# Kernel optimization log

Hardware: AMD Instinct MI355X
Metric: run time of the kernel (lower is better)

Reference implementation:

```python
import jax, jax.numpy as jnp
import numpy as np

N = 100000
IN_DIM = 128
HID = 64
OUT = 4


def _gcn_conv(x, W, b, src, dst, deg_inv_sqrt):
    """PyG GCNConv: linear transform, then symmetric-normalized scatter-add.
    src/dst already include self-loops; deg_inv_sqrt precomputed over them."""
    h = x @ W                                   # [N, H]
    norm = deg_inv_sqrt[src] * deg_inv_sqrt[dst]  # [E+N]
    msg = h[src] * norm[:, None]                # gather + scale, [E+N, H]
    out = jax.ops.segment_sum(msg, dst, num_segments=N)  # scatter-add
    return out + b


def setup_inputs() -> dict:
    key = jax.random.key(0)
    ks = jax.random.split(key, 8)
    E = 1600000
    x = jax.random.normal(ks[0], (N, IN_DIM), dtype=jnp.float32)
    edge_index = jax.random.randint(ks[1], (2, E), 0, N, dtype=jnp.int32)
    # Glorot-ish init for weights
    W1 = jax.random.normal(ks[2], (IN_DIM, HID), dtype=jnp.float32) / np.sqrt(IN_DIM)
    b1 = jnp.zeros((HID,), dtype=jnp.float32)
    W2 = jax.random.normal(ks[3], (HID, HID), dtype=jnp.float32) / np.sqrt(HID)
    b2 = jnp.zeros((HID,), dtype=jnp.float32)
    Wfc = jax.random.normal(ks[4], (HID, OUT), dtype=jnp.float32) / np.sqrt(HID)
    bfc = jnp.zeros((OUT,), dtype=jnp.float32)
    return {"x": x, "edge_index": edge_index, "W1": W1, "b1": b1,
            "W2": W2, "b2": b2, "Wfc": Wfc, "bfc": bfc}


def reference(x, edge_index, W1, b1, W2, b2, Wfc, bfc):
    # Add self-loops (GCNConv default add_self_loops=True)
    loops = jnp.arange(N, dtype=edge_index.dtype)
    src = jnp.concatenate([edge_index[0], loops])
    dst = jnp.concatenate([edge_index[1], loops])
    # Symmetric normalization: deg computed at aggregation targets (dst)
    deg = jax.ops.segment_sum(jnp.ones_like(dst, dtype=x.dtype), dst,
                              num_segments=N)
    deg_inv_sqrt = jnp.where(deg > 0, jax.lax.rsqrt(deg), 0.0)

    h = _gcn_conv(x, W1, b1, src, dst, deg_inv_sqrt)
    h = jax.nn.relu(h)                 # dropout is identity in eval mode
    h = _gcn_conv(h, W2, b2, src, dst, deg_inv_sqrt)
    h = jax.nn.relu(h)
    return h @ Wfc + bfc               # [N, 4]
```

## Files before the change

kernel.cpp:

```cpp
#include <hip/hip_runtime.h>
#include <hip/hip_fp16.h>


#define BCAP 5120
#define BINB 512
#define CHUNK 3200

typedef float v2f __attribute__((ext_vector_type(2)));
typedef _Float16 f16x8 __attribute__((ext_vector_type(8)));
typedef float f32x4 __attribute__((ext_vector_type(4)));

__global__ __launch_bounds__(256) void k_prep(const float* __restrict__ W1,
                                              const float* __restrict__ W2,
                                              _Float16* __restrict__ wt1,
                                              _Float16* __restrict__ wt2,
                                              int* __restrict__ bcur) {
    int gid = threadIdx.x + blockIdx.x * blockDim.x;
    {
        int k = gid >> 6, nn = gid & 63;
        wt1[nn * 136 + k] = (_Float16)W1[gid];
    }
    if (gid < 64 * 64) {
        int k = gid >> 6, nn = gid & 63;
        wt2[nn * 72 + k] = (_Float16)W2[gid];
    }
    if (gid < 512) bcur[gid] = 0;
}

__global__ __launch_bounds__(256) void k_bin(const int* __restrict__ src,
                                             const int* __restrict__ dst, int e,
                                             int* bcur, unsigned* __restrict__ binned) {
    __shared__ unsigned ec[CHUNK];
    __shared__ unsigned short eb[CHUNK];
    __shared__ int lh[512], lbase[512], lr[512];
    int t = threadIdx.x;
    for (int i = t; i < 512; i += 256) { lh[i] = 0; lr[i] = 0; }
    __syncthreads();
    int chunk = (e + gridDim.x - 1) / gridDim.x;
    int lo = blockIdx.x * chunk;
    int hi = min(e, lo + chunk);
    for (int i = lo + t; i < hi; i += 256) {
        int d = dst[i];
        int b = d >> 8;
        ec[i - lo] = ((unsigned)src[i] << 8) | (unsigned)(d & 255);
        eb[i - lo] = (unsigned short)b;
        atomicAdd(&lh[b], 1);
    }
    __syncthreads();
    for (int i = t; i < 512; i += 256)
        lbase[i] = lh[i] ? atomicAdd(&bcur[i], lh[i]) : 0;
    __syncthreads();
    int cnt = hi - lo;
    for (int i = t; i < cnt; i += 256) {
        int b = eb[i];
        int r = lbase[b] + atomicAdd(&lr[b], 1);
        if (r < BCAP)
            binned[(size_t)b * BCAP + r] = ec[i];
    }
}

__global__ __launch_bounds__(256) void k_bucket(const unsigned* __restrict__ binned,
                                                const int* __restrict__ bcur,
                                                int n, int* __restrict__ offs,
                                                int* __restrict__ cnt,
                                                float* __restrict__ dis,
                                                int* __restrict__ csr) {
    __shared__ unsigned ec[BCAP];
    __shared__ int nh[256], nsc[256], nr[256];
    int b = blockIdx.x, t = threadIdx.x;
    int node0 = b << 8;
    size_t ebase = (size_t)b * BCAP;
    int ecnt = min(bcur[b], BCAP);
    nh[t] = 0; nr[t] = 0;
    __syncthreads();
    for (int j = t; j < ecnt; j += 256) {
        unsigned ed = binned[ebase + j];
        ec[j] = ed;
        atomicAdd(&nh[ed & 255u], 1);
    }
    __syncthreads();
    int v = nh[t];
    nsc[t] = v;
    __syncthreads();
    for (int o = 1; o < 256; o <<= 1) {
        int x = (t >= o) ? nsc[t - o] : 0;
        __syncthreads();
        nsc[t] += x;
        __syncthreads();
    }
    int ex = nsc[t] - v;
    int d = node0 + t;
    if (d < n) {
        offs[d] = (int)ebase + ex;
        cnt[d]  = v;
        dis[d]  = rsqrtf((float)(v + 1));
    }
    nsc[t] = ex;
    __syncthreads();
    for (int j = t; j < ecnt; j += 256) {
        unsigned ed = ec[j];
        int ld = ed & 255u;
        int r = atomicAdd(&nr[ld], 1);
        csr[ebase + nsc[ld] + r] = (int)(ed >> 8);
    }
}

template<int K, typename TI>
__global__ __launch_bounds__(256) void k_gemm_mfma(const TI* __restrict__ X,
                                                   const _Float16* __restrict__ Wt,
                                                   const float* __restrict__ dis,
                                                   __half* __restrict__ Hh, int n) {
    constexpr int KP = K + 8;
    __shared__ _Float16 As[128 * KP];
    __shared__ _Float16 Bs[64 * KP];

    int t = threadIdx.x;
    _Float16* H = (_Float16*)Hh;

    constexpr int NF4 = 64 * KP / 8;
    for (int i = t; i < NF4; i += 256)
        ((float4*)Bs)[i] = ((const float4*)Wt)[i];

    int row0 = blockIdx.x * 128;
    if (sizeof(TI) == 4) {
        const float* Xf = (const float*)X;
        #pragma unroll
        for (int p = 0; p < 8; ++p) {
            int gi  = t + p * 256;
            int row = gi >> 4, sg = gi & 15;
            int grow = row0 + row;
            float4 v0 = make_float4(0.f, 0.f, 0.f, 0.f), v1 = v0;
            if (grow < n) {
                v0 = *(const float4*)(Xf + (size_t)grow * K + sg * 8);
                v1 = *(const float4*)(Xf + (size_t)grow * K + sg * 8 + 4);
            }
            union { __half2 h[4]; float4 f; } u;
            u.h[0] = __floats2half2_rn(v0.x, v0.y);
            u.h[1] = __floats2half2_rn(v0.z, v0.w);
            u.h[2] = __floats2half2_rn(v1.x, v1.y);
            u.h[3] = __floats2half2_rn(v1.z, v1.w);
            *(float4*)(As + row * KP + sg * 8) = u.f;
        }
    } else {
        const __half* Xh = (const __half*)X;
        #pragma unroll
        for (int p = 0; p < 4; ++p) {
            int gi  = t + p * 256;
            int row = gi >> 3, sg = gi & 7;
            int grow = row0 + row;
            float4 v = make_float4(0.f, 0.f, 0.f, 0.f);
            if (grow < n)
                v = *(const float4*)(Xh + (size_t)grow * K + sg * 8);
            *(float4*)(As + row * KP + sg * 8) = v;
        }
    }
    __syncthreads();

    int wv   = t >> 6;
    int lane = t & 63;
    int m    = lane & 15;
    int quad = lane >> 4;
    int r0   = wv * 32;

    f32x4 acc[2][4] = {};
    #pragma unroll
    for (int kb = 0; kb < K / 32; ++kb) {
        f16x8 af0 = *(const f16x8*)(As + (r0 + m) * KP + quad * 8 + kb * 32);
        f16x8 af1 = *(const f16x8*)(As + (r0 + 16 + m) * KP + quad * 8 + kb * 32);
        #pragma unroll
        for (int nt = 0; nt < 4; ++nt) {
            f16x8 bf = *(const f16x8*)(Bs + (nt * 16 + m) * KP + quad * 8 + kb * 32);
            acc[0][nt] = __builtin_amdgcn_mfma_f32_16x16x32_f16(af0, bf, acc[0][nt], 0, 0, 0);
            acc[1][nt] = __builtin_amdgcn_mfma_f32_16x16x32_f16(af1, bf, acc[1][nt], 0, 0, 0);
        }
    }

    #pragma unroll
    for (int mt = 0; mt < 2; ++mt) {
        float dv[4]; int gr[4];
        #pragma unroll
        for (int r = 0; r < 4; ++r) {
            gr[r] = row0 + r0 + mt * 16 + quad * 4 + r;
            dv[r] = (gr[r] < n) ? dis[gr[r]] : 0.f;
        }
        #pragma unroll
        for (int nt = 0; nt < 4; ++nt)
            #pragma unroll
            for (int r = 0; r < 4; ++r) {
                if (gr[r] < n)
                    H[(size_t)gr[r] * 64 + nt * 16 + m] =
                        (_Float16)(acc[mt][nt][r] * dv[r]);
                else if (gr[r] == n)
                    H[(size_t)n * 64 + nt * 16 + m] = (_Float16)0.f;
            }
    }
}

__device__ inline void add_row(const __half* __restrict__ hp, int s, int c4,
                               v2f& lo, v2f& hi) {
    float2 raw = *(const float2*)(hp + (size_t)s * 64 + c4);
    const __half2* p = (const __half2*)&raw;
    float2 l = __half22float2(p[0]);
    float2 h = __half22float2(p[1]);
    lo += (v2f){ l.x, l.y };
    hi += (v2f){ h.x, h.y };
}

template<bool FUSE>
__global__ __launch_bounds__(256) void k_gather(const __half* __restrict__ hp,
                                                const int* __restrict__ csr,
                                                const int* __restrict__ off,
                                                const int* __restrict__ cnt,
                                                const float* __restrict__ dis,
                                                const float* __restrict__ bias,
                                                void* __restrict__ outb,
                                                const float* __restrict__ Wfc,
                                                const float* __restrict__ bfc,
                                                int n) {
    int lane = threadIdx.x & 63;
    int wid  = (blockIdx.x * blockDim.x + threadIdx.x) >> 6;
    if (wid >= n) return;
    int d    = wid;
    int esub = lane >> 4;
    int c4   = (lane & 15) * 4;

    int start = off[d], num = cnt[d];
    int idx = (lane < num) ? csr[start + lane] : 0;
    int lim = min(num, 64);

    v2f aL[4] = {}, aH[4] = {};
    if (esub == 0)
        add_row(hp, d, c4, aL[0], aH[0]);

    int j = 0;
    for (; j + 16 <= lim; j += 16) {
        int s0 = __shfl(idx, j + esub);
        int s1 = __shfl(idx, j + 4 + esub);
        int s2 = __shfl(idx, j + 8 + esub);
        int s3 = __shfl(idx, j + 12 + esub);
        add_row(hp, s0, c4, aL[0], aH[0]);
        add_row(hp, s1, c4, aL[1], aH[1]);
        add_row(hp, s2, c4, aL[2], aH[2]);
        add_row(hp, s3, c4, aL[3], aH[3]);
    }
    for (; j < lim; j += 4) {
        int jj = j + esub;
        int sr = __shfl(idx, jj);
        int s  = (jj < lim) ? sr : n;
        add_row(hp, s, c4, aL[0], aH[0]);
    }
    for (int j2 = 64; j2 < num; j2 += 4) {
        int jj = j2 + esub;
        if (jj < num) {
            int s = csr[start + jj];
            add_row(hp, s, c4, aL[1], aH[1]);
        }
    }
    v2f sL = (aL[0] + aL[1]) + (aL[2] + aL[3]);
    v2f sH = (aH[0] + aH[1]) + (aH[2] + aH[3]);
    float4 a0 = make_float4(sL.x, sL.y, sH.x, sH.y);
    #pragma unroll
    for (int o = 16; o <= 32; o <<= 1) {
        a0.x += __shfl_xor(a0.x, o);
        a0.y += __shfl_xor(a0.y, o);
        a0.z += __shfl_xor(a0.z, o);
        a0.w += __shfl_xor(a0.w, o);
    }
    float dd = dis[d];
    float4 bb = *(const float4*)(bias + c4);
    float4 o;
    o.x = fmaxf(bb.x + dd * a0.x, 0.f);
    o.y = fmaxf(bb.y + dd * a0.y, 0.f);
    o.z = fmaxf(bb.z + dd * a0.z, 0.f);
    o.w = fmaxf(bb.w + dd * a0.w, 0.f);
    if (!FUSE) {
        if (esub == 0) {
            union { __half2 h[2]; float2 f; } u;
            u.h[0] = __floats2half2_rn(o.x, o.y);
            u.h[1] = __floats2half2_rn(o.z, o.w);
            *(float2*)((__half*)outb + (size_t)d * 64 + c4) = u.f;
        }
    } else {
        const float4* W4 = (const float4*)Wfc;
        float4 w0 = W4[c4 + 0], w1 = W4[c4 + 1], w2 = W4[c4 + 2], w3 = W4[c4 + 3];
        float4 p;
        p.x = o.x * w0.x + o.y * w1.x + o.z * w2.x + o.w * w3.x;
        p.y = o.x * w0.y + o.y * w1.y + o.z * w2.y + o.w * w3.y;
        p.z = o.x * w0.z + o.y * w1.z + o.z * w2.z + o.w * w3.z;
        p.w = o.x * w0.w + o.y * w1.w + o.z * w2.w + o.w * w3.w;
        #pragma unroll
        for (int q = 1; q <= 8; q <<= 1) {
            p.x += __shfl_xor(p.x, q);
            p.y += __shfl_xor(p.y, q);
            p.z += __shfl_xor(p.z, q);
            p.w += __shfl_xor(p.w, q);
        }
        if (lane == 0) {
            float4 bf = *(const float4*)bfc;
            float4 r = make_float4(p.x + bf.x, p.y + bf.y, p.z + bf.z, p.w + bf.w);
            ((float4*)outb)[d] = r;
        }
    }
}

static inline size_t align256(size_t x) { return (x + 255) & ~(size_t)255; }

extern "C" void kernel_launch(void* const* d_in, const int* in_sizes, int n_in,
                              void* d_out, int out_size, void* d_ws, size_t ws_size,
                              hipStream_t stream) {
    const float* x   = (const float*)d_in[0];
    const int*   ei  = (const int*)d_in[1];
    const float* W1  = (const float*)d_in[2];
    const float* b1  = (const float*)d_in[3];
    const float* W2  = (const float*)d_in[4];
    const float* b2  = (const float*)d_in[5];
    const float* Wfc = (const float*)d_in[6];
    const float* bfc = (const float*)d_in[7];
    float* out = (float*)d_out;

    int n = in_sizes[0] / 128;
    int e = in_sizes[1] / 2;
    const int* src = ei;
    const int* dst = ei + e;

    char* ws = (char*)d_ws;
    size_t p = 0;
    float*    dis    = (float*)   (ws + p); p = align256(p + (size_t)n * 4);
    int*      counts = (int*)     (ws + p); p = align256(p + (size_t)n * 4);
    int*      offs   = (int*)     (ws + p); p = align256(p + (size_t)n * 4);
    int*      bcur   = (int*)     (ws + p); p = align256(p + 512 * 4);
    _Float16* wt1    = (_Float16*)(ws + p); p = align256(p + 64 * 136 * 2);
    _Float16* wt2    = (_Float16*)(ws + p); p = align256(p + 64 * 72 * 2);
    int*      csr    = (int*)     (ws + p); p = align256(p + (size_t)512 * BCAP * 4);
    unsigned* binned = (unsigned*)(ws + p); p = align256(p + (size_t)512 * BCAP * 4);
    __half*   hbuf   = (__half*)  (ws + p); p = align256(p + (size_t)(n + 1) * 64 * 2);
    __half*   a1h    = (__half*)  (ws + p);

    int gb  = (n + 127) / 128;
    int nbk = (n + 255) / 256;

    k_prep<<<32, 256, 0, stream>>>(W1, W2, wt1, wt2, bcur);
    k_bin<<<BINB, 256, 0, stream>>>(src, dst, e, bcur, binned);
    k_bucket<<<nbk, 256, 0, stream>>>(binned, bcur, n, offs, counts, dis, csr);

    k_gemm_mfma<128, float><<<gb, 256, 0, stream>>>(x, wt1, dis, hbuf, n);
    k_gather<false><<<(n * 64 + 255) / 256, 256, 0, stream>>>(
        hbuf, csr, offs, counts, dis, b1, a1h, nullptr, nullptr, n);

    k_gemm_mfma<64, __half><<<gb, 256, 0, stream>>>(a1h, wt2, dis, hbuf, n);
    k_gather<true><<<(n * 64 + 255) / 256, 256, 0, stream>>>(
        hbuf, csr, offs, counts, dis, b2, out, Wfc, bfc, n);
}
```

Measured before the change: 264.9 us.

## Fuse second-layer GEMM into first gather and shrink node buckets to 128

The layer-2 linear transform (64x64 matmul with W2, pre-scaled by deg_inv_sqrt) is folded into the epilogue of the first aggregation kernel using cross-lane shuffles, so the separate MFMA GEMM launch and its intermediate activation buffer round-trip are removed. Node bins are also halved to 128 nodes each (1024 bins, smaller capacity) so the bucket kernel runs more blocks with less shared memory. The fused epilogue does 64 FMAs per lane in fp32 on vector ALUs with per-lane W2 loads, which adds work to a memory-bound gather kernel. The smaller bin capacity gives less headroom for skewed degree distributions.

```diff
diff --git a/kernel.cpp b/kernel.cpp
--- a/kernel.cpp
+++ b/kernel.cpp
@@ -2,29 +2,26 @@
 #include <hip/hip_fp16.h>
 
 
-#define BCAP 5120
+#define BCAP 2816
 #define BINB 512
 #define CHUNK 3200
+#define NBKT 782
 
 typedef float v2f __attribute__((ext_vector_type(2)));
 typedef _Float16 f16x8 __attribute__((ext_vector_type(8)));
 typedef float f32x4 __attribute__((ext_vector_type(4)));
 
 __global__ __launch_bounds__(256) void k_prep(const float* __restrict__ W1,
-                                              const float* __restrict__ W2,
                                               _Float16* __restrict__ wt1,
-                                              _Float16* __restrict__ wt2,
-                                              int* __restrict__ bcur) {
+                                              int* __restrict__ bcur,
+                                              __half* __restrict__ h2, int n) {
     int gid = threadIdx.x + blockIdx.x * blockDim.x;
     {
         int k = gid >> 6, nn = gid & 63;
         wt1[nn * 136 + k] = (_Float16)W1[gid];
     }
-    if (gid < 64 * 64) {
-        int k = gid >> 6, nn = gid & 63;
-        wt2[nn * 72 + k] = (_Float16)W2[gid];
-    }
-    if (gid < 512) bcur[gid] = 0;
+    if (gid < 1024) bcur[gid] = 0;
+    if (gid < 64) h2[(size_t)n * 64 + gid] = __half(0.f);
 }
 
 __global__ __launch_bounds__(256) void k_bin(const int* __restrict__ src,
@@ -32,22 +29,22 @@
                                              int* bcur, unsigned* __restrict__ binned) {
     __shared__ unsigned ec[CHUNK];
     __shared__ unsigned short eb[CHUNK];
-    __shared__ int lh[512], lbase[512], lr[512];
+    __shared__ int lh[1024], lbase[1024], lr[1024];
     int t = threadIdx.x;
-    for (int i = t; i < 512; i += 256) { lh[i] = 0; lr[i] = 0; }
+    for (int i = t; i < 1024; i += 256) { lh[i] = 0; lr[i] = 0; }
     __syncthreads();
     int chunk = (e + gridDim.x - 1) / gridDim.x;
     int lo = blockIdx.x * chunk;
     int hi = min(e, lo + chunk);
     for (int i = lo + t; i < hi; i += 256) {
         int d = dst[i];
-        int b = d >> 8;
-        ec[i - lo] = ((unsigned)src[i] << 8) | (unsigned)(d & 255);
+        int b = d >> 7;
+        ec[i - lo] = ((unsigned)src[i] << 7) | (unsigned)(d & 127);
         eb[i - lo] = (unsigned short)b;
         atomicAdd(&lh[b], 1);
     }
     __syncthreads();
-    for (int i = t; i < 512; i += 256)
+    for (int i = t; i < 1024; i += 256)
         lbase[i] = lh[i] ? atomicAdd(&bcur[i], lh[i]) : 0;
     __syncthreads();
     int cnt = hi - lo;
@@ -66,51 +63,52 @@
                                                 float* __restrict__ dis,
                                                 int* __restrict__ csr) {
     __shared__ unsigned ec[BCAP];
-    __shared__ int nh[256], nsc[256], nr[256];
+    __shared__ int nh[128], nsc[128], nr[128];
     int b = blockIdx.x, t = threadIdx.x;
-    int node0 = b << 8;
+    int node0 = b << 7;
     size_t ebase = (size_t)b * BCAP;
     int ecnt = min(bcur[b], BCAP);
-    nh[t] = 0; nr[t] = 0;
+    if (t < 128) { nh[t] = 0; nr[t] = 0; }
     __syncthreads();
     for (int j = t; j < ecnt; j += 256) {
         unsigned ed = binned[ebase + j];
         ec[j] = ed;
-        atomicAdd(&nh[ed & 255u], 1);
-    }
-    __syncthreads();
-    int v = nh[t];
-    nsc[t] = v;
-    __syncthreads();
-    for (int o = 1; o < 256; o <<= 1) {
-        int x = (t >= o) ? nsc[t - o] : 0;
+        atomicAdd(&nh[ed & 127u], 1);
+    }
+    __syncthreads();
+    int v = (t < 128) ? nh[t] : 0;
+    if (t < 128) nsc[t] = v;
+    __syncthreads();
+    for (int o = 1; o < 128; o <<= 1) {
+        int x = (t >= o && t < 128) ? nsc[t - o] : 0;
         __syncthreads();
-        nsc[t] += x;
+        if (t < 128) nsc[t] += x;
         __syncthreads();
     }
-    int ex = nsc[t] - v;
-    int d = node0 + t;
-    if (d < n) {
-        offs[d] = (int)ebase + ex;
-        cnt[d]  = v;
-        dis[d]  = rsqrtf((float)(v + 1));
-    }
-    nsc[t] = ex;
+    if (t < 128) {
+        int ex = nsc[t] - v;
+        int d = node0 + t;
+        if (d < n) {
+            offs[d] = (int)ebase + ex;
+            cnt[d]  = v;
+            dis[d]  = rsqrtf((float)(v + 1));
+        }
+        nsc[t] = ex;
+    }
     __syncthreads();
     for (int j = t; j < ecnt; j += 256) {
         unsigned ed = ec[j];
-        int ld = ed & 255u;
+        int ld = ed & 127u;
         int r = atomicAdd(&nr[ld], 1);
-        csr[ebase + nsc[ld] + r] = (int)(ed >> 8);
-    }
-}
-
-template<int K, typename TI>
-__global__ __launch_bounds__(256) void k_gemm_mfma(const TI* __restrict__ X,
+        csr[ebase + nsc[ld] + r] = (int)(ed >> 7);
+    }
+}
+
+__global__ __launch_bounds__(256) void k_gemm_mfma(const float* __restrict__ X,
                                                    const _Float16* __restrict__ Wt,
                                                    const float* __restrict__ dis,
                                                    __half* __restrict__ Hh, int n) {
-    constexpr int KP = K + 8;
+    constexpr int K = 128, KP = K + 8;
     __shared__ _Float16 As[128 * KP];
     __shared__ _Float16 Bs[64 * KP];
 
@@ -122,37 +120,22 @@
         ((float4*)Bs)[i] = ((const float4*)Wt)[i];
 
     int row0 = blockIdx.x * 128;
-    if (sizeof(TI) == 4) {
-        const float* Xf = (const float*)X;
-        #pragma unroll
-        for (int p = 0; p < 8; ++p) {
-            int gi  = t + p * 256;
-            int row = gi >> 4, sg = gi & 15;
-            int grow = row0 + row;
-            float4 v0 = make_float4(0.f, 0.f, 0.f, 0.f), v1 = v0;
-            if (grow < n) {
-                v0 = *(const float4*)(Xf + (size_t)grow * K + sg * 8);
-                v1 = *(const float4*)(Xf + (size_t)grow * K + sg * 8 + 4);
-            }
-            union { __half2 h[4]; float4 f; } u;
-            u.h[0] = __floats2half2_rn(v0.x, v0.y);
-            u.h[1] = __floats2half2_rn(v0.z, v0.w);
-            u.h[2] = __floats2half2_rn(v1.x, v1.y);
-            u.h[3] = __floats2half2_rn(v1.z, v1.w);
-            *(float4*)(As + row * KP + sg * 8) = u.f;
-        }
-    } else {
-        const __half* Xh = (const __half*)X;
-        #pragma unroll
-        for (int p = 0; p < 4; ++p) {
-            int gi  = t + p * 256;
-            int row = gi >> 3, sg = gi & 7;
-            int grow = row0 + row;
-            float4 v = make_float4(0.f, 0.f, 0.f, 0.f);
-            if (grow < n)
-                v = *(const float4*)(Xh + (size_t)grow * K + sg * 8);
-            *(float4*)(As + row * KP + sg * 8) = v;
-        }
+    #pragma unroll
+    for (int p = 0; p < 8; ++p) {
+        int gi  = t + p * 256;
+        int row = gi >> 4, sg = gi & 15;
+        int grow = row0 + row;
+        float4 v0 = make_float4(0.f, 0.f, 0.f, 0.f), v1 = v0;
+        if (grow < n) {
+            v0 = *(const float4*)(X + (size_t)grow * K + sg * 8);
+            v1 = *(const float4*)(X + (size_t)grow * K + sg * 8 + 4);
+        }
+        union { __half2 h[4]; float4 f; } u;
+        u.h[0] = __floats2half2_rn(v0.x, v0.y);
+        u.h[1] = __floats2half2_rn(v0.z, v0.w);
+        u.h[2] = __floats2half2_rn(v1.x, v1.y);
+        u.h[3] = __floats2half2_rn(v1.z, v1.w);
+        *(float4*)(As + row * KP + sg * 8) = u.f;
     }
     __syncthreads();
 
@@ -206,7 +189,7 @@
     hi += (v2f){ h.x, h.y };
 }
 
-template<bool FUSE>
+template<int MODE>
 __global__ __launch_bounds__(256) void k_gather(const __half* __restrict__ hp,
                                                 const int* __restrict__ csr,
                                                 const int* __restrict__ off,
@@ -214,7 +197,7 @@
                                                 const float* __restrict__ dis,
                                                 const float* __restrict__ bias,
                                                 void* __restrict__ outb,
-                                                const float* __restrict__ Wfc,
+                                                const float* __restrict__ Wx,
                                                 const float* __restrict__ bfc,
                                                 int n) {
     int lane = threadIdx.x & 63;
@@ -273,15 +256,39 @@
     o.y = fmaxf(bb.y + dd * a0.y, 0.f);
     o.z = fmaxf(bb.z + dd * a0.z, 0.f);
     o.w = fmaxf(bb.w + dd * a0.w, 0.f);
-    if (!FUSE) {
+
+    if (MODE == 1) {
+        float4 p = make_float4(0.f, 0.f, 0.f, 0.f);
+        #pragma unroll
+        for (int jj = 0; jj < 16; ++jj) {
+            int k = esub * 16 + jj;
+            int srcl = k >> 2;
+            float av;
+            switch (jj & 3) {
+                case 0: av = __shfl(o.x, srcl); break;
+                case 1: av = __shfl(o.y, srcl); break;
+                case 2: av = __shfl(o.z, srcl); break;
+                default: av = __shfl(o.w, srcl); break;
+            }
+            float4 wr = *(const float4*)(Wx + k * 64 + c4);
+            p.x += av * wr.x; p.y += av * wr.y;
+            p.z += av * wr.z; p.w += av * wr.w;
+        }
+        #pragma unroll
+        for (int q = 16; q <= 32; q <<= 1) {
+            p.x += __shfl_xor(p.x, q);
+            p.y += __shfl_xor(p.y, q);
+            p.z += __shfl_xor(p.z, q);
+            p.w += __shfl_xor(p.w, q);
+        }
         if (esub == 0) {
             union { __half2 h[2]; float2 f; } u;
-            u.h[0] = __floats2half2_rn(o.x, o.y);
-            u.h[1] = __floats2half2_rn(o.z, o.w);
+            u.h[0] = __floats2half2_rn(p.x * dd, p.y * dd);
+            u.h[1] = __floats2half2_rn(p.z * dd, p.w * dd);
             *(float2*)((__half*)outb + (size_t)d * 64 + c4) = u.f;
         }
     } else {
-        const float4* W4 = (const float4*)Wfc;
+        const float4* W4 = (const float4*)Wx;
         float4 w0 = W4[c4 + 0], w1 = W4[c4 + 1], w2 = W4[c4 + 2], w3 = W4[c4 + 3];
         float4 p;
         p.x = o.x * w0.x + o.y * w1.x + o.z * w2.x + o.w * w3.x;
@@ -328,26 +335,22 @@
     float*    dis    = (float*)   (ws + p); p = align256(p + (size_t)n * 4);
     int*      counts = (int*)     (ws + p); p = align256(p + (size_t)n * 4);
     int*      offs   = (int*)     (ws + p); p = align256(p + (size_t)n * 4);
-    int*      bcur   = (int*)     (ws + p); p = align256(p + 512 * 4);
+    int*      bcur   = (int*)     (ws + p); p = align256(p + 1024 * 4);
     _Float16* wt1    = (_Float16*)(ws + p); p = align256(p + 64 * 136 * 2);
-    _Float16* wt2    = (_Float16*)(ws + p); p = align256(p + 64 * 72 * 2);
-    int*      csr    = (int*)     (ws + p); p = align256(p + (size_t)512 * BCAP * 4);
-    unsigned* binned = (unsigned*)(ws + p); p = align256(p + (size_t)512 * BCAP * 4);
+    int*      csr    = (int*)     (ws + p); p = align256(p + (size_t)1024 * BCAP * 4);
+    unsigned* binned = (unsigned*)(ws + p); p = align256(p + (size_t)1024 * BCAP * 4);
     __half*   hbuf   = (__half*)  (ws + p); p = align256(p + (size_t)(n + 1) * 64 * 2);
-    __half*   a1h    = (__half*)  (ws + p);
-
-    int gb  = (n + 127) / 128;
-    int nbk = (n + 255) / 256;
-
-    k_prep<<<32, 256, 0, stream>>>(W1, W2, wt1, wt2, bcur);
+    __half*   h2buf  = (__half*)  (ws + p);
+
+    int gb = (n + 127) / 128;
+
+    k_prep<<<32, 256, 0, stream>>>(W1, wt1, bcur, h2buf, n);
     k_bin<<<BINB, 256, 0, stream>>>(src, dst, e, bcur, binned);
-    k_bucket<<<nbk, 256, 0, stream>>>(binned, bcur, n, offs, counts, dis, csr);
-
-    k_gemm_mfma<128, float><<<gb, 256, 0, stream>>>(x, wt1, dis, hbuf, n);
-    k_gather<false><<<(n * 64 + 255) / 256, 256, 0, stream>>>(
-        hbuf, csr, offs, counts, dis, b1, a1h, nullptr, nullptr, n);
-
-    k_gemm_mfma<64, __half><<<gb, 256, 0, stream>>>(a1h, wt2, dis, hbuf, n);
-    k_gather<true><<<(n * 64 + 255) / 256, 256, 0, stream>>>(
-        hbuf, csr, offs, counts, dis, b2, out, Wfc, bfc, n);
-}
+    k_bucket<<<NBKT, 256, 0, stream>>>(binned, bcur, n, offs, counts, dis, csr);
+
+    k_gemm_mfma<<<gb, 256, 0, stream>>>(x, wt1, dis, hbuf, n);
+    k_gather<1><<<(n * 64 + 255) / 256, 256, 0, stream>>>(
+        hbuf, csr, offs, counts, dis, b1, h2buf, W2, nullptr, n);
+    k_gather<2><<<(n * 64 + 255) / 256, 256, 0, stream>>>(
+        h2buf, csr, offs, counts, dis, b2, out, Wfc, bfc, n);
+}
```

New measurement: 278.7 us. +5.2%, slower.
